# Kernel optimization log

Measured on AMD Instinct MI355X. Metric: run time of the kernel, lower is better.

The kernel has to match this reference:

```python
import jax, jax.numpy as jnp
import numpy as np

B, NUM_RX, NUM_CHIRPS, SAMPLES = 16, 4, 64, 256
D_BINS, R_BINS = 64, 256


def _conv3d(x, w, b, pad):
    y = jax.lax.conv_general_dilated(x, w, (1, 1, 1), pad,
                                     dimension_numbers=('NCDHW', 'OIDHW', 'NCDHW'))
    return y + b[None, :, None, None, None]


def _conv2d(x, w, b, pad):
    y = jax.lax.conv_general_dilated(x, w, (1, 1), pad,
                                     dimension_numbers=('NCHW', 'OIHW', 'NCHW'))
    return y + b[None, :, None, None]


def _bn2(x, s, t):
    return x * s[None, :, None, None] + t[None, :, None, None]


def _bn3(x, s, t):
    return x * s[None, :, None, None, None] + t[None, :, None, None, None]


def _upsample_bilinear_ac(x, oh, ow):
    # torch Upsample(mode='bilinear', align_corners=True)
    _, _, h, w = x.shape
    ph = jnp.linspace(0.0, h - 1.0, oh)
    pw = jnp.linspace(0.0, w - 1.0, ow)
    h0 = jnp.clip(jnp.floor(ph).astype(jnp.int32), 0, h - 1)
    h1 = jnp.clip(h0 + 1, 0, h - 1)
    fh = ph - h0
    w0 = jnp.clip(jnp.floor(pw).astype(jnp.int32), 0, w - 1)
    w1 = jnp.clip(w0 + 1, 0, w - 1)
    fw = pw - w0
    x = x[:, :, h0, :] * (1.0 - fh)[None, None, :, None] + x[:, :, h1, :] * fh[None, None, :, None]
    x = x[:, :, :, w0] * (1.0 - fw) + x[:, :, :, w1] * fw
    return x


def setup_inputs() -> dict:
    ks = iter(jax.random.split(jax.random.key(0), 80))

    def nrm(shape, s=0.05):
        return s * jax.random.normal(next(ks), shape, dtype=jnp.float32)

    inp = {'x': jax.random.normal(next(ks), (B, NUM_RX, NUM_CHIRPS, SAMPLES, 2), dtype=jnp.float32)}

    def conv(name, shape):
        inp[name + '_w'] = nrm(shape)
        inp[name + '_b'] = nrm((shape[0],))

    def bn(name, n):  # BatchNorm in inference form folded to scale/shift
        inp[name + '_s'] = 1.0 + nrm((n,), 0.1)
        inp[name + '_t'] = nrm((n,), 0.1)

    conv('tc1', (16, 2, 1, 1, 3)); bn('tc1', 16)
    conv('tc2', (32, 16, 1, 1, 3)); bn('tc2', 32)
    conv('rx', (32, 32, NUM_RX, 1, 1)); bn('rx', 32)
    conv('cc1', (64, 32 * NUM_CHIRPS, 3, 3)); bn('cc1', 64)
    conv('cc2', (64, 64, 3, 3)); bn('cc2', 64)
    conv('rd1', (128, 64, 3, 3)); bn('rd1', 128)
    conv('rd2', (128, 128, 3, 3)); bn('rd2', 128)
    conv('up1', (64, 128, 3, 3)); bn('up1', 64)
    conv('up2', (32, 64, 3, 3)); bn('up2', 32)
    conv('up3', (1, 32, 1, 1))
    inp['wr'] = jax.random.normal(next(ks), (SAMPLES, R_BINS, 2), dtype=jnp.float32)
    inp['wd'] = jax.random.normal(next(ks), (NUM_CHIRPS, D_BINS, 2), dtype=jnp.float32)
    return inp


def reference(x, tc1_w, tc1_b, tc1_s, tc1_t, tc2_w, tc2_b, tc2_s, tc2_t,
              rx_w, rx_b, rx_s, rx_t, cc1_w, cc1_b, cc1_s, cc1_t,
              cc2_w, cc2_b, cc2_s, cc2_t, rd1_w, rd1_b, rd1_s, rd1_t,
              rd2_w, rd2_b, rd2_s, rd2_t, up1_w, up1_b, up1_s, up1_t,
              up2_w, up2_b, up2_s, up2_t, up3_w, up3_b, wr, wd):
    r = jax.nn.relu
    p3 = [(0, 0), (0, 0), (1, 1)]
    p2 = [(1, 1), (1, 1)]
    h = jnp.transpose(x, (0, 4, 1, 2, 3))                      # [B,2,RX,C,S]
    h = r(_bn3(_conv3d(h, tc1_w, tc1_b, p3), tc1_s, tc1_t))
    h = r(_bn3(_conv3d(h, tc2_w, tc2_b, p3), tc2_s, tc2_t))
    h = r(_bn3(_conv3d(h, rx_w, rx_b, [(0, 0)] * 3), rx_s, rx_t))[:, :, 0]  # [B,32,C,S]
    h = h.reshape(h.shape[0], -1, SAMPLES)[:, :, None, :]      # [B,32*C,1,S]
    h = r(_bn2(_conv2d(h, cc1_w, cc1_b, p2), cc1_s, cc1_t))
    h = r(_bn2(_conv2d(h, cc2_w, cc2_b, p2), cc2_s, cc2_t))
    h = r(_bn2(_conv2d(h, rd1_w, rd1_b, p2), rd1_s, rd1_t))
    h = r(_bn2(_conv2d(h, rd2_w, rd2_b, p2), rd2_s, rd2_t))
    h = _upsample_bilinear_ac(h, D_BINS, R_BINS)               # [B,128,D,R]
    h = r(_bn2(_conv2d(h, up1_w, up1_b, p2), up1_s, up1_t))
    h = r(_bn2(_conv2d(h, up2_w, up2_b, p2), up2_s, up2_t))
    h = jax.nn.sigmoid(_conv2d(h, up3_w, up3_b, [(0, 0), (0, 0)]))  # [B,1,D,R]
    # learnable_fft (input is real: x_imag = 0), loops -> two batched matmuls
    xr = h[:, 0]                                               # [B,D,R]
    rr = jnp.einsum('bcs,sr->bcr', xr, wr[:, :, 0])            # range DFT, real
    ri = jnp.einsum('bcs,sr->bcr', xr, wr[:, :, 1])            # range DFT, imag
    rdr = jnp.einsum('bcr,cd->bdr', rr, wd[:, :, 0]) - jnp.einsum('bcr,cd->bdr', ri, wd[:, :, 1])
    rdi = jnp.einsum('bcr,cd->bdr', rr, wd[:, :, 1]) + jnp.einsum('bcr,cd->bdr', ri, wd[:, :, 0])
    mag = jnp.sqrt(rdr * rdr + rdi * rdi) / (NUM_CHIRPS * SAMPLES)
    out = jnp.clip(h + 0.1 * mag[:, None], 0.0, 1.0)
    return jnp.transpose(out, (0, 2, 3, 1))                    # [B,D,R,1]
```

## Files before the change

kernel.cpp:

```cpp
#include <hip/hip_runtime.h>
#include <math.h>

#define OFF_A      0u
#define OFF_P      8388608u
#define OFF_WCC1   10485760u
#define OFF_BCC1   11010048u
#define OFF_WCC2   11010112u
#define OFF_BCC2   11026496u
#define OFF_WRD1   11026560u
#define OFF_BRD1   11059328u
#define OFF_WRD2   11059456u
#define OFF_BRD2   11124992u
#define OFF_WUP1   11125120u
#define OFF_BUP1   11223424u
#define OFF_WUP2   11223488u
#define OFF_BUP2   11346368u
#define OFF_WRX    11346400u
#define OFF_R      0u
#define OFF_U1     524288u
#define OFF_H      1310720u

__device__ __forceinline__ void fma4(float4& a, const float4& x, float w) {
  a.x = fmaf(x.x, w, a.x); a.y = fmaf(x.y, w, a.y);
  a.z = fmaf(x.z, w, a.z); a.w = fmaf(x.w, w, a.w);
}

__global__ __launch_bounds__(256) void k_repack(
    const float* __restrict__ rx_w, const float* __restrict__ rx_s,
    const float* __restrict__ cc1_w, const float* __restrict__ cc1_b, const float* __restrict__ cc1_s, const float* __restrict__ cc1_t,
    const float* __restrict__ cc2_w, const float* __restrict__ cc2_b, const float* __restrict__ cc2_s, const float* __restrict__ cc2_t,
    const float* __restrict__ rd1_w, const float* __restrict__ rd1_b, const float* __restrict__ rd1_s, const float* __restrict__ rd1_t,
    const float* __restrict__ rd2_w, const float* __restrict__ rd2_b, const float* __restrict__ rd2_s, const float* __restrict__ rd2_t,
    const float* __restrict__ up1_w, const float* __restrict__ up1_b, const float* __restrict__ up1_s, const float* __restrict__ up1_t,
    const float* __restrict__ up2_w, const float* __restrict__ up2_b, const float* __restrict__ up2_s, const float* __restrict__ up2_t,
    float* __restrict__ ws)
{
  const int tid = blockIdx.x * blockDim.x + threadIdx.x;
  const int nth = gridDim.x * blockDim.x;

  for (int i = tid; i < 4096; i += nth) {
    int oc = i & 31, ic = (i >> 5) & 31, rxi = i >> 10;
    ws[OFF_WRX + i] = rx_w[(oc*32 + ic)*4 + rxi] * rx_s[oc];
  }

  for (int i = tid; i < 2048*64*4; i += nth) {
    int k = i & 3, oc = (i >> 2) & 63, c2 = i >> 8;
    ws[OFF_WCC1 + i] = (k < 3) ? cc1_w[((oc*2048 + c2)*3 + 1)*3 + k] * cc1_s[oc] : 0.f;
  }
  for (int i = tid; i < 64; i += nth) ws[OFF_BCC1 + i] = cc1_b[i]*cc1_s[i] + cc1_t[i];

  for (int i = tid; i < 64*64*4; i += nth) {
    int k = i & 3, oc = (i >> 2) & 63, ic = i >> 8;
    ws[OFF_WCC2 + i] = (k < 3) ? cc2_w[((oc*64 + ic)*3 + 1)*3 + k] * cc2_s[oc] : 0.f;
  }
  for (int i = tid; i < 64; i += nth) ws[OFF_BCC2 + i] = cc2_b[i]*cc2_s[i] + cc2_t[i];

  for (int i = tid; i < 64*128*4; i += nth) {
    int k = i & 3, oc = (i >> 2) & 127, ic = i >> 9;
    ws[OFF_WRD1 + i] = (k < 3) ? rd1_w[((oc*64 + ic)*3 + 1)*3 + k] * rd1_s[oc] : 0.f;
  }
  for (int i = tid; i < 128; i += nth) ws[OFF_BRD1 + i] = rd1_b[i]*rd1_s[i] + rd1_t[i];

  for (int i = tid; i < 128*128*4; i += nth) {
    int k = i & 3, oc = (i >> 2) & 127, ic = i >> 9;
    ws[OFF_WRD2 + i] = (k < 3) ? rd2_w[((oc*128 + ic)*3 + 1)*3 + k] * rd2_s[oc] : 0.f;
  }
  for (int i = tid; i < 128; i += nth) ws[OFF_BRD2 + i] = rd2_b[i]*rd2_s[i] + rd2_t[i];

  for (int i = tid; i < 3*128*64*4; i += nth) {
    int k = i & 3, oc = (i >> 2) & 63, ic = (i >> 8) & 127, v = i >> 15;
    float val = 0.f;
    if (k < 3) {
      const int m = (v == 0) ? 6 : (v == 1) ? 7 : 3;
      float a = 0.f;
      for (int kh = 0; kh < 3; ++kh)
        if ((m >> kh) & 1) a += up1_w[((oc*128 + ic)*3 + kh)*3 + k];
      val = a * up1_s[oc];
    }
    ws[OFF_WUP1 + i] = val;
  }
  for (int i = tid; i < 64; i += nth) ws[OFF_BUP1 + i] = up1_b[i]*up1_s[i] + up1_t[i];

  for (int i = tid; i < 5*3*64*32*4; i += nth) {
    int k = i & 3, oc = (i >> 2) & 31, ic = (i >> 7) & 63, t = i >> 13;
    int src = t % 3, v = t / 3;
    float val = 0.f;
    if (k < 3) {
      const int MASKS[15] = {2,4,0,  1,6,0,  0,7,0,  0,3,4,  0,1,2};
      const int m = MASKS[v*3 + src];
      float a = 0.f;
      for (int kh = 0; kh < 3; ++kh)
        if ((m >> kh) & 1) a += up2_w[((oc*64 + ic)*3 + kh)*3 + k];
      val = a * up2_s[oc];
    }
    ws[OFF_WUP2 + i] = val;
  }
  for (int i = tid; i < 32; i += nth) ws[OFF_BUP2 + i] = up2_b[i]*up2_s[i] + up2_t[i];
}

__global__ __launch_bounds__(256) void k_front(
    const float* __restrict__ x,
    const float* __restrict__ w1, const float* __restrict__ b1, const float* __restrict__ s1, const float* __restrict__ t1bn,
    const float* __restrict__ w2, const float* __restrict__ b2, const float* __restrict__ s2, const float* __restrict__ t2bn,
    const float* __restrict__ wrxF, const float* __restrict__ brx, const float* __restrict__ srx, const float* __restrict__ trx,
    float* __restrict__ A)
{
  __shared__ __align__(16) float t1s[16][256];
  __shared__ __align__(16) float t2s[16][256];
  __shared__ __align__(16) float w1f[16][6];
  __shared__ float b1f[16];
  __shared__ __align__(16) float w2t[16][3][32];
  __shared__ float b2f[32];
  __shared__ float brxf[32];

  const int tid = threadIdx.x;
  const int b = blockIdx.x >> 6, chirp = blockIdx.x & 63;

  if (tid < 96) (&w1f[0][0])[tid] = w1[tid] * s1[tid/6];
  if (tid < 16) b1f[tid] = b1[tid]*s1[tid] + t1bn[tid];
  for (int i = tid; i < 1536; i += 256) {
    int oc = i / 48, r = i - oc*48, ic = r / 3, k = r - ic*3;
    w2t[ic][k][oc] = w2[i] * s2[oc];
  }
  if (tid < 32) b2f[tid] = b2[tid]*s2[tid] + t2bn[tid];
  if (tid < 32) brxf[tid] = brx[tid]*srx[tid] + trx[tid];
  __syncthreads();

  const int s  = tid;
  const int sg = tid & 63;
  const int q  = tid >> 6;
  const int s0 = sg * 4;

  float4 acc[8];
  #pragma unroll
  for (int j = 0; j < 8; ++j) acc[j] = make_float4(0.f, 0.f, 0.f, 0.f);

  #pragma unroll 1
  for (int rxi = 0; rxi < 4; ++rxi) {
    {
      const float2* xb2 = (const float2*)(x + ((size_t)(((b*4 + rxi)*64 + chirp)*256) << 1));
      float2 xm = xb2[s];
      float2 xl = xb2[(s == 0) ? 0 : (s - 1)];
      float2 xr = xb2[(s == 255) ? 255 : (s + 1)];
      if (s == 0)   { xl.x = 0.f; xl.y = 0.f; }
      if (s == 255) { xr.x = 0.f; xr.y = 0.f; }
      #pragma unroll 4
      for (int o = 0; o < 16; ++o) {
        float v = b1f[o];
        v = fmaf(xl.x, w1f[o][0], v);
        v = fmaf(xm.x, w1f[o][1], v);
        v = fmaf(xr.x, w1f[o][2], v);
        v = fmaf(xl.y, w1f[o][3], v);
        v = fmaf(xm.y, w1f[o][4], v);
        v = fmaf(xr.y, w1f[o][5], v);
        t1s[o][s] = fmaxf(v, 0.f);
      }
    }
    __syncthreads();

    #pragma unroll 1
    for (int h = 0; h < 2; ++h) {
      {
        const int ocb = h*16 + q*4;
        float4 t2a[4];
        #pragma unroll
        for (int j = 0; j < 4; ++j) {
          float bv = b2f[ocb + j];
          t2a[j] = make_float4(bv, bv, bv, bv);
        }
        #pragma unroll 4
        for (int ic = 0; ic < 16; ++ic) {
          float4 tm = *(const float4*)&t1s[ic][s0];
          float tl = t1s[ic][(sg == 0) ? 0 : (s0 - 1)];
          float tr = t1s[ic][(sg == 63) ? 255 : (s0 + 4)];
          if (sg == 0)  tl = 0.f;
          if (sg == 63) tr = 0.f;
          float4 win0 = make_float4(tl, tm.x, tm.y, tm.z);
          float4 win2 = make_float4(tm.y, tm.z, tm.w, tr);
          float4 wA = *(const float4*)&w2t[ic][0][ocb];
          float4 wB = *(const float4*)&w2t[ic][1][ocb];
          float4 wC = *(const float4*)&w2t[ic][2][ocb];
          fma4(t2a[0], win0, wA.x); fma4(t2a[0], tm, wB.x); fma4(t2a[0], win2, wC.x);
          fma4(t2a[1], win0, wA.y); fma4(t2a[1], tm, wB.y); fma4(t2a[1], win2, wC.y);
          fma4(t2a[2], win0, wA.z); fma4(t2a[2], tm, wB.z); fma4(t2a[2], win2, wC.z);
          fma4(t2a[3], win0, wA.w); fma4(t2a[3], tm, wB.w); fma4(t2a[3], win2, wC.w);
        }
        #pragma unroll
        for (int j = 0; j < 4; ++j) {
          float4 r;
          r.x = fmaxf(t2a[j].x, 0.f); r.y = fmaxf(t2a[j].y, 0.f);
          r.z = fmaxf(t2a[j].z, 0.f); r.w = fmaxf(t2a[j].w, 0.f);
          *(float4*)&t2s[q*4 + j][s0] = r;
        }
      }
      __syncthreads();

      {
        const float* wbase = wrxF + ((rxi*32 + h*16)*32) + q*8;
        #pragma unroll 8
        for (int ic = 0; ic < 16; ++ic) {
          float4 tv = *(const float4*)&t2s[ic][s0];
          float4 wa = *(const float4*)(wbase + ic*32);
          float4 wb = *(const float4*)(wbase + ic*32 + 4);
          fma4(acc[0], tv, wa.x); fma4(acc[1], tv, wa.y);
          fma4(acc[2], tv, wa.z); fma4(acc[3], tv, wa.w);
          fma4(acc[4], tv, wb.x); fma4(acc[5], tv, wb.y);
          fma4(acc[6], tv, wb.z); fma4(acc[7], tv, wb.w);
        }
      }
      __syncthreads();
    }
  }

  #pragma unroll
  for (int j = 0; j < 8; ++j) {
    int oc = q*8 + j;
    float bb = brxf[oc];
    float4 r;
    r.x = fmaxf(acc[j].x + bb, 0.f); r.y = fmaxf(acc[j].y + bb, 0.f);
    r.z = fmaxf(acc[j].z + bb, 0.f); r.w = fmaxf(acc[j].w + bb, 0.f);
    *(float4*)&A[(size_t)((b*2048 + oc*64 + chirp)*256) + s0] = r;
  }
}

__global__ __launch_bounds__(256) void k_cc1(
    const float* __restrict__ A, const float* __restrict__ wp, float* __restrict__ P)
{
  __shared__ __align__(16) float As[256][36];
  const int tid = threadIdx.x;
  const int ks = blockIdx.x & 7;
  const int stile = (blockIdx.x >> 3) & 7;
  const int b = blockIdx.x >> 6;
  const int s0 = stile * 32;
  const int oc = tid & 63;
  const int sg = tid >> 6;
  const int cbase = ks * 256;
  const float4* w4 = (const float4*)wp;

  for (int i = tid; i < 256*36; i += 256) {
    int c = i / 36, si = i - c*36;
    int sA = s0 - 1 + si;
    float v = 0.f;
    if (si < 34 && sA >= 0 && sA < 256)
      v = A[(size_t)(b*2048 + cbase + c)*256 + sA];
    As[c][si] = v;
  }
  __syncthreads();

  const int sb = sg * 8;
  float4 acc0 = make_float4(0.f,0.f,0.f,0.f);
  float4 acc1 = make_float4(0.f,0.f,0.f,0.f);
  #pragma unroll 4
  for (int c = 0; c < 256; ++c) {
    float4 w = w4[(size_t)(cbase + c)*64 + oc];
    float4 a0 = *(const float4*)&As[c][sb];
    float4 a1 = *(const float4*)&As[c][sb + 4];
    float2 a2 = *(const float2*)&As[c][sb + 8];
    acc0.x = fmaf(a0.x,w.x, fmaf(a0.y,w.y, fmaf(a0.z,w.z, acc0.x)));
    acc0.y = fmaf(a0.y,w.x, fmaf(a0.z,w.y, fmaf(a0.w,w.z, acc0.y)));
    acc0.z = fmaf(a0.z,w.x, fmaf(a0.w,w.y, fmaf(a1.x,w.z, acc0.z)));
    acc0.w = fmaf(a0.w,w.x, fmaf(a1.x,w.y, fmaf(a1.y,w.z, acc0.w)));
    acc1.x = fmaf(a1.x,w.x, fmaf(a1.y,w.y, fmaf(a1.z,w.z, acc1.x)));
    acc1.y = fmaf(a1.y,w.x, fmaf(a1.z,w.y, fmaf(a1.w,w.z, acc1.y)));
    acc1.z = fmaf(a1.z,w.x, fmaf(a1.w,w.y, fmaf(a2.x,w.z, acc1.z)));
    acc1.w = fmaf(a1.w,w.x, fmaf(a2.x,w.y, fmaf(a2.y,w.z, acc1.w)));
  }
  float* Pk = P + ((size_t)(ks*16 + b)*256)*64;
  int s = s0 + sb;
  Pk[(size_t)(s+0)*64 + oc] = acc0.x;
  Pk[(size_t)(s+1)*64 + oc] = acc0.y;
  Pk[(size_t)(s+2)*64 + oc] = acc0.z;
  Pk[(size_t)(s+3)*64 + oc] = acc0.w;
  Pk[(size_t)(s+4)*64 + oc] = acc1.x;
  Pk[(size_t)(s+5)*64 + oc] = acc1.y;
  Pk[(size_t)(s+6)*64 + oc] = acc1.z;
  Pk[(size_t)(s+7)*64 + oc] = acc1.w;
}

__global__ __launch_bounds__(256) void k_mid(
    const float* __restrict__ P, const float* __restrict__ bcc1,
    const float* __restrict__ wcc2, const float* __restrict__ bcc2,
    const float* __restrict__ wrd1, const float* __restrict__ brd1,
    const float* __restrict__ wrd2, const float* __restrict__ brd2,
    float* __restrict__ R)
{
  __shared__ float c1s[14][64];
  __shared__ float c2s[14][64];
  __shared__ float r1s[10][128];
  const int tid = threadIdx.x;
  const int b = blockIdx.x >> 5;
  const int s0 = (blockIdx.x & 31) * 8;
  const float4* wc2 = (const float4*)wcc2;
  const float4* wr1 = (const float4*)wrd1;
  const float4* wr2 = (const float4*)wrd2;

  for (int i = tid; i < 14*64; i += 256) {
    int si = i >> 6, ic = i & 63;
    int sA = s0 - 3 + si;
    float v = 0.f;
    if (sA >= 0 && sA < 256) {
      float a = bcc1[ic];
      #pragma unroll
      for (int ksp = 0; ksp < 8; ++ksp)
        a += P[((size_t)(ksp*16 + b)*256 + sA)*64 + ic];
      v = fmaxf(a, 0.f);
    }
    c1s[si][ic] = v;
  }
  __syncthreads();

  {
    const int g = tid >> 6, oc = tid & 63;
    if (g < 3) {
      float4 acc;
      float bb = bcc2[oc];
      acc = make_float4(bb, bb, bb, bb);
      for (int ic = 0; ic < 64; ++ic) {
        float4 w = wc2[ic*64 + oc];
        float c0 = c1s[g*4+0][ic], c1 = c1s[g*4+1][ic], c2 = c1s[g*4+2][ic];
        float c3 = c1s[g*4+3][ic], c4 = c1s[g*4+4][ic], c5 = c1s[g*4+5][ic];
        acc.x = fmaf(c0,w.x, fmaf(c1,w.y, fmaf(c2,w.z, acc.x)));
        acc.y = fmaf(c1,w.x, fmaf(c2,w.y, fmaf(c3,w.z, acc.y)));
        acc.z = fmaf(c2,w.x, fmaf(c3,w.y, fmaf(c4,w.z, acc.z)));
        acc.w = fmaf(c3,w.x, fmaf(c4,w.y, fmaf(c5,w.z, acc.w)));
      }
      c2s[g*4+0][oc] = fmaxf(acc.x, 0.f);
      c2s[g*4+1][oc] = fmaxf(acc.y, 0.f);
      c2s[g*4+2][oc] = fmaxf(acc.z, 0.f);
      c2s[g*4+3][oc] = fmaxf(acc.w, 0.f);
    } else {
      int k = tid - 192;
      c2s[12][k] = 0.f;
      c2s[13][k] = 0.f;
    }
  }
  __syncthreads();

  for (int it = tid; it < 384; it += 256) {
    const int oc = it & 127, g = it >> 7;
    float4 acc;
    float bb = brd1[oc];
    acc = make_float4(bb, bb, bb, bb);
    for (int ic = 0; ic < 64; ++ic) {
      float4 w = wr1[ic*128 + oc];
      float c0 = c2s[g*4+0][ic], c1 = c2s[g*4+1][ic], c2 = c2s[g*4+2][ic];
      float c3 = c2s[g*4+3][ic], c4 = c2s[g*4+4][ic], c5 = c2s[g*4+5][ic];
      acc.x = fmaf(c0,w.x, fmaf(c1,w.y, fmaf(c2,w.z, acc.x)));
      acc.y = fmaf(c1,w.x, fmaf(c2,w.y, fmaf(c3,w.z, acc.y)));
      acc.z = fmaf(c2,w.x, fmaf(c3,w.y, fmaf(c4,w.z, acc.z)));
      acc.w = fmaf(c3,w.x, fmaf(c4,w.y, fmaf(c5,w.z, acc.w)));
    }
    r1s[g*4+0][oc] = fmaxf(acc.x, 0.f);
    r1s[g*4+1][oc] = fmaxf(acc.y, 0.f);
    if (g < 2) {
      r1s[g*4+2][oc] = fmaxf(acc.z, 0.f);
      r1s[g*4+3][oc] = fmaxf(acc.w, 0.f);
    }
  }
  __syncthreads();

  {
    const int g = tid >> 7, oc = tid & 127;
    float4 acc;
    float bb = brd2[oc];
    acc = make_float4(bb, bb, bb, bb);
    for (int ic = 0; ic < 128; ++ic) {
      float4 w = wr2[ic*128 + oc];
      float c0 = r1s[g*4+0][ic], c1 = r1s[g*4+1][ic], c2 = r1s[g*4+2][ic];
      float c3 = r1s[g*4+3][ic], c4 = r1s[g*4+4][ic], c5 = r1s[g*4+5][ic];
      acc.x = fmaf(c0,w.x, fmaf(c1,w.y, fmaf(c2,w.z, acc.x)));
      acc.y = fmaf(c1,w.x, fmaf(c2,w.y, fmaf(c3,w.z, acc.y)));
      acc.z = fmaf(c2,w.x, fmaf(c3,w.y, fmaf(c4,w.z, acc.z)));
      acc.w = fmaf(c3,w.x, fmaf(c4,w.y, fmaf(c5,w.z, acc.w)));
    }
    int s = s0 + g*4;
    R[((size_t)b*256 + s+0)*128 + oc] = fmaxf(acc.x, 0.f);
    R[((size_t)b*256 + s+1)*128 + oc] = fmaxf(acc.y, 0.f);
    R[((size_t)b*256 + s+2)*128 + oc] = fmaxf(acc.z, 0.f);
    R[((size_t)b*256 + s+3)*128 + oc] = fmaxf(acc.w, 0.f);
  }
}

__global__ __launch_bounds__(192) void k_up1(
    const float* __restrict__ R, const float* __restrict__ wup1, const float* __restrict__ bup1,
    float* __restrict__ U1)
{
  __shared__ float Rs[10][128];
  const int tid = threadIdx.x;
  const int b = blockIdx.x >> 5;
  const int s0 = (blockIdx.x & 31) * 8;
  for (int i = tid; i < 10*128; i += 192) {
    int si = i >> 7, ic = i & 127;
    int sA = s0 - 1 + si;
    Rs[si][ic] = (sA >= 0 && sA < 256) ? R[((size_t)b*256 + sA)*128 + ic] : 0.f;
  }
  __syncthreads();
  const int vi = tid >> 6, oc = tid & 63;
  const float4* w4 = (const float4*)wup1;
  float acc[8];
  float bb = bup1[oc];
  #pragma unroll
  for (int j = 0; j < 8; ++j) acc[j] = bb;
  for (int ic = 0; ic < 128; ++ic) {
    float4 w = w4[(vi*128 + ic)*64 + oc];
    float r0 = Rs[0][ic], r1 = Rs[1][ic], r2 = Rs[2][ic], r3 = Rs[3][ic], r4 = Rs[4][ic];
    float r5 = Rs[5][ic], r6 = Rs[6][ic], r7 = Rs[7][ic], r8 = Rs[8][ic], r9 = Rs[9][ic];
    acc[0] = fmaf(r0,w.x, fmaf(r1,w.y, fmaf(r2,w.z, acc[0])));
    acc[1] = fmaf(r1,w.x, fmaf(r2,w.y, fmaf(r3,w.z, acc[1])));
    acc[2] = fmaf(r2,w.x, fmaf(r3,w.y, fmaf(r4,w.z, acc[2])));
    acc[3] = fmaf(r3,w.x, fmaf(r4,w.y, fmaf(r5,w.z, acc[3])));
    acc[4] = fmaf(r4,w.x, fmaf(r5,w.y, fmaf(r6,w.z, acc[4])));
    acc[5] = fmaf(r5,w.x, fmaf(r6,w.y, fmaf(r7,w.z, acc[5])));
    acc[6] = fmaf(r6,w.x, fmaf(r7,w.y, fmaf(r8,w.z, acc[6])));
    acc[7] = fmaf(r7,w.x, fmaf(r8,w.y, fmaf(r9,w.z, acc[7])));
  }
  #pragma unroll
  for (int j = 0; j < 8; ++j)
    U1[((size_t)(b*3 + vi)*256 + s0 + j)*64 + oc] = fmaxf(acc[j], 0.f);
}

__global__ __launch_bounds__(192) void k_up2(
    const float* __restrict__ U1, const float* __restrict__ wup2, const float* __restrict__ bup2,
    const float* __restrict__ up3_w, const float* __restrict__ up3_b,
    float* __restrict__ H)
{
  __shared__ float u1s[3][10][64];
  __shared__ float u2s[5][32][9];
  const int tid = threadIdx.x;
  const int b = blockIdx.x >> 5;
  const int s0 = (blockIdx.x & 31) * 8;
  for (int i = tid; i < 3*10*64; i += 192) {
    int v = i / 640, r = i - v*640, si = r >> 6, ic = r & 63;
    int sA = s0 - 1 + si;
    u1s[v][si][ic] = (sA >= 0 && sA < 256) ? U1[((size_t)(b*3 + v)*256 + sA)*64 + ic] : 0.f;
  }
  __syncthreads();
  if (tid < 160) {
    const int v = tid >> 5, oc = tid & 31;
    const float4* w4 = (const float4*)wup2;
    float acc[8];
    float bb = bup2[oc];
    #pragma unroll
    for (int j = 0; j < 8; ++j) acc[j] = bb;
    for (int src = 0; src < 3; ++src)
      for (int ic = 0; ic < 64; ++ic) {
        float4 w = w4[((v*3 + src)*64 + ic)*32 + oc];
        float r0 = u1s[src][0][ic], r1 = u1s[src][1][ic], r2 = u1s[src][2][ic];
        float r3 = u1s[src][3][ic], r4 = u1s[src][4][ic], r5 = u1s[src][5][ic];
        float r6 = u1s[src][6][ic], r7 = u1s[src][7][ic], r8 = u1s[src][8][ic];
        float r9 = u1s[src][9][ic];
        acc[0] = fmaf(r0,w.x, fmaf(r1,w.y, fmaf(r2,w.z, acc[0])));
        acc[1] = fmaf(r1,w.x, fmaf(r2,w.y, fmaf(r3,w.z, acc[1])));
        acc[2] = fmaf(r2,w.x, fmaf(r3,w.y, fmaf(r4,w.z, acc[2])));
        acc[3] = fmaf(r3,w.x, fmaf(r4,w.y, fmaf(r5,w.z, acc[3])));
        acc[4] = fmaf(r4,w.x, fmaf(r5,w.y, fmaf(r6,w.z, acc[4])));
        acc[5] = fmaf(r5,w.x, fmaf(r6,w.y, fmaf(r7,w.z, acc[5])));
        acc[6] = fmaf(r6,w.x, fmaf(r7,w.y, fmaf(r8,w.z, acc[6])));
        acc[7] = fmaf(r7,w.x, fmaf(r8,w.y, fmaf(r9,w.z, acc[7])));
      }
    #pragma unroll
    for (int j = 0; j < 8; ++j) u2s[v][oc][j] = fmaxf(acc[j], 0.f);
  }
  __syncthreads();
  if (tid < 40) {
    int v = tid >> 3, j = tid & 7;
    float a = up3_b[0];
    for (int ic = 0; ic < 32; ++ic)
      a = fmaf(u2s[v][ic][j], up3_w[ic], a);
    H[(size_t)(b*5 + v)*256 + s0 + j] = 1.f / (1.f + expf(-a));
  }
}

__global__ __launch_bounds__(64) void k_spec(
    const float* __restrict__ H, const float* __restrict__ wr, const float* __restrict__ wd,
    float* __restrict__ out)
{
  __shared__ float hs[5][256];
  __shared__ float S0[64], S1[64];
  __shared__ float wds[4][64][2];
  const int tid = threadIdx.x;
  const int b = blockIdx.x >> 2;
  const int rt = blockIdx.x & 3;
  for (int i = tid; i < 1280; i += 64) hs[i >> 8][i & 255] = H[(size_t)b*1280 + i];
  {
    float a0 = 0.f, a1 = 0.f;
    for (int c = 2; c <= 61; ++c) {
      a0 += wd[(c*64 + tid)*2 + 0];
      a1 += wd[(c*64 + tid)*2 + 1];
    }
    S0[tid] = a0; S1[tid] = a1;
  }
  for (int i = tid; i < 512; i += 64) {
    int row = i >> 7, rem = i & 127, d = rem >> 1, comp = rem & 1;
    int c = (row < 2) ? row : (60 + row);
    wds[row][d][comp] = wd[(c*64 + d)*2 + comp];
  }
  __syncthreads();
  const int r = rt*64 + tid;
  float rr0=0,rr1=0,rr2=0,rr3=0,rr4=0, ri0=0,ri1=0,ri2=0,ri3=0,ri4=0;
  const float2* wr2p = (const float2*)wr;
  for (int s = 0; s < 256; ++s) {
    float2 w = wr2p[s*256 + r];
    float h0 = hs[0][s], h1 = hs[1][s], h2 = hs[2][s], h3 = hs[3][s], h4 = hs[4][s];
    rr0 = fmaf(h0, w.x, rr0); ri0 = fmaf(h0, w.y, ri0);
    rr1 = fmaf(h1, w.x, rr1); ri1 = fmaf(h1, w.y, ri1);
    rr2 = fmaf(h2, w.x, rr2); ri2 = fmaf(h2, w.y, ri2);
    rr3 = fmaf(h3, w.x, rr3); ri3 = fmaf(h3, w.y, ri3);
    rr4 = fmaf(h4, w.x, rr4); ri4 = fmaf(h4, w.y, ri4);
  }
  for (int d = 0; d < 64; ++d) {
    float w0r = wds[0][d][0], w0i = wds[0][d][1];
    float w1r = wds[1][d][0], w1i = wds[1][d][1];
    float w2r = wds[2][d][0], w2i = wds[2][d][1];
    float w3r = wds[3][d][0], w3i = wds[3][d][1];
    float s0v = S0[d], s1v = S1[d];
    float rdr = rr0*w0r + rr1*w1r + rr2*s0v + rr3*w2r + rr4*w3r
              - ri0*w0i - ri1*w1i - ri2*s1v - ri3*w2i - ri4*w3i;
    float rdi = rr0*w0i + rr1*w1i + rr2*s1v + rr3*w2i + rr4*w3i
              + ri0*w0r + ri1*w1r + ri2*s0v + ri3*w2r + ri4*w3r;
    float mag = sqrtf(rdr*rdr + rdi*rdi) * (1.0f / 16384.0f);
    int v = (d == 0) ? 0 : (d == 1) ? 1 : (d <= 61) ? 2 : ((d == 62) ? 3 : 4);
    float o = hs[v][r] + 0.1f * mag;
    out[(size_t)b*16384 + d*256 + r] = fminf(fmaxf(o, 0.f), 1.f);
  }
}

extern "C" void kernel_launch(void* const* d_in, const int* in_sizes, int n_in,
                              void* d_out, int out_size, void* d_ws, size_t ws_size,
                              hipStream_t stream)
{
  const float* x     = (const float*)d_in[0];
  const float* tc1_w = (const float*)d_in[1];  const float* tc1_b = (const float*)d_in[2];
  const float* tc1_s = (const float*)d_in[3];  const float* tc1_t = (const float*)d_in[4];
  const float* tc2_w = (const float*)d_in[5];  const float* tc2_b = (const float*)d_in[6];
  const float* tc2_s = (const float*)d_in[7];  const float* tc2_t = (const float*)d_in[8];
  const float* rx_w  = (const float*)d_in[9];  const float* rx_b  = (const float*)d_in[10];
  const float* rx_s  = (const float*)d_in[11]; const float* rx_t  = (const float*)d_in[12];
  const float* cc1_w = (const float*)d_in[13]; const float* cc1_b = (const float*)d_in[14];
  const float* cc1_s = (const float*)d_in[15]; const float* cc1_t = (const float*)d_in[16];
  const float* cc2_w = (const float*)d_in[17]; const float* cc2_b = (const float*)d_in[18];
  const float* cc2_s = (const float*)d_in[19]; const float* cc2_t = (const float*)d_in[20];
  const float* rd1_w = (const float*)d_in[21]; const float* rd1_b = (const float*)d_in[22];
  const float* rd1_s = (const float*)d_in[23]; const float* rd1_t = (const float*)d_in[24];
  const float* rd2_w = (const float*)d_in[25]; const float* rd2_b = (const float*)d_in[26];
  const float* rd2_s = (const float*)d_in[27]; const float* rd2_t = (const float*)d_in[28];
  const float* up1_w = (const float*)d_in[29]; const float* up1_b = (const float*)d_in[30];
  const float* up1_s = (const float*)d_in[31]; const float* up1_t = (const float*)d_in[32];
  const float* up2_w = (const float*)d_in[33]; const float* up2_b = (const float*)d_in[34];
  const float* up2_s = (const float*)d_in[35]; const float* up2_t = (const float*)d_in[36];
  const float* up3_w = (const float*)d_in[37]; const float* up3_b = (const float*)d_in[38];
  const float* wr    = (const float*)d_in[39];
  const float* wd    = (const float*)d_in[40];
  float* ws  = (float*)d_ws;
  float* out = (float*)d_out;

  k_repack<<<1024, 256, 0, stream>>>(rx_w, rx_s,
                                     cc1_w, cc1_b, cc1_s, cc1_t,
                                     cc2_w, cc2_b, cc2_s, cc2_t,
                                     rd1_w, rd1_b, rd1_s, rd1_t,
                                     rd2_w, rd2_b, rd2_s, rd2_t,
                                     up1_w, up1_b, up1_s, up1_t,
                                     up2_w, up2_b, up2_s, up2_t, ws);
  k_front<<<1024, 256, 0, stream>>>(x, tc1_w, tc1_b, tc1_s, tc1_t,
                                    tc2_w, tc2_b, tc2_s, tc2_t,
                                    ws + OFF_WRX, rx_b, rx_s, rx_t, ws + OFF_A);
  k_cc1<<<1024, 256, 0, stream>>>(ws + OFF_A, ws + OFF_WCC1, ws + OFF_P);
  k_mid<<<512, 256, 0, stream>>>(ws + OFF_P, ws + OFF_BCC1,
                                 ws + OFF_WCC2, ws + OFF_BCC2,
                                 ws + OFF_WRD1, ws + OFF_BRD1,
                                 ws + OFF_WRD2, ws + OFF_BRD2, ws + OFF_R);
  k_up1<<<512, 192, 0, stream>>>(ws + OFF_R, ws + OFF_WUP1, ws + OFF_BUP1, ws + OFF_U1);
  k_up2<<<512, 192, 0, stream>>>(ws + OFF_U1, ws + OFF_WUP2, ws + OFF_BUP2, up3_w, up3_b, ws + OFF_H);
  k_spec<<<64, 64, 0, stream>>>(ws + OFF_H, wr, wd, out);
}
```

Baseline: 420.4 us.

## Restructure k_front to per-thread register tiles with uniform weight loads

Moves the tc1/tc2/rx weight and bias folding into k_repack so k_front no longer prepares weights in shared memory per block. Each thread now owns one sample and keeps all 32 tc2 outputs and 32 rx accumulators in registers, reading weights from global memory with wave-uniform addresses (scalar loads) instead of staging t2 through shared memory. This removes the t2s shared buffer and several barriers per rxi iteration, at the cost of higher register pressure and scalar-load traffic. It also sets launch_bounds(256,4).

Measured after the change: 392.7 us. 1.07x faster.

```diff
diff --git a/kernel.cpp b/kernel.cpp
--- a/kernel.cpp
+++ b/kernel.cpp
@@ -16,6 +16,11 @@
 #define OFF_WUP2   11223488u
 #define OFF_BUP2   11346368u
 #define OFF_WRX    11346400u
+#define OFF_W1F    11350496u
+#define OFF_B1F    11350592u
+#define OFF_W2F    11350608u
+#define OFF_B2F    11352144u
+#define OFF_BRXF   11352176u
 #define OFF_R      0u
 #define OFF_U1     524288u
 #define OFF_H      1310720u
@@ -26,7 +31,9 @@
 }
 
 __global__ __launch_bounds__(256) void k_repack(
-    const float* __restrict__ rx_w, const float* __restrict__ rx_s,
+    const float* __restrict__ tc1_w, const float* __restrict__ tc1_b, const float* __restrict__ tc1_s, const float* __restrict__ tc1_t,
+    const float* __restrict__ tc2_w, const float* __restrict__ tc2_b, const float* __restrict__ tc2_s, const float* __restrict__ tc2_t,
+    const float* __restrict__ rx_w, const float* __restrict__ rx_b, const float* __restrict__ rx_s, const float* __restrict__ rx_t,
     const float* __restrict__ cc1_w, const float* __restrict__ cc1_b, const float* __restrict__ cc1_s, const float* __restrict__ cc1_t,
     const float* __restrict__ cc2_w, const float* __restrict__ cc2_b, const float* __restrict__ cc2_s, const float* __restrict__ cc2_t,
     const float* __restrict__ rd1_w, const float* __restrict__ rd1_b, const float* __restrict__ rd1_s, const float* __restrict__ rd1_t,
@@ -38,10 +45,18 @@
   const int tid = blockIdx.x * blockDim.x + threadIdx.x;
   const int nth = gridDim.x * blockDim.x;
 
+  for (int i = tid; i < 96; i += nth) ws[OFF_W1F + i] = tc1_w[i] * tc1_s[i/6];
+  for (int i = tid; i < 16; i += nth) ws[OFF_B1F + i] = tc1_b[i]*tc1_s[i] + tc1_t[i];
+  for (int i = tid; i < 1536; i += nth) {
+    int oc = i & 31, r = i >> 5, k = r % 3, ic = r / 3;
+    ws[OFF_W2F + i] = tc2_w[oc*48 + ic*3 + k] * tc2_s[oc];
+  }
+  for (int i = tid; i < 32; i += nth) ws[OFF_B2F + i] = tc2_b[i]*tc2_s[i] + tc2_t[i];
   for (int i = tid; i < 4096; i += nth) {
     int oc = i & 31, ic = (i >> 5) & 31, rxi = i >> 10;
     ws[OFF_WRX + i] = rx_w[(oc*32 + ic)*4 + rxi] * rx_s[oc];
   }
+  for (int i = tid; i < 32; i += nth) ws[OFF_BRXF + i] = rx_b[i]*rx_s[i] + rx_t[i];
 
   for (int i = tid; i < 2048*64*4; i += nth) {
     int k = i & 3, oc = (i >> 2) & 63, c2 = i >> 8;
@@ -98,42 +113,26 @@
   for (int i = tid; i < 32; i += nth) ws[OFF_BUP2 + i] = up2_b[i]*up2_s[i] + up2_t[i];
 }
 
-__global__ __launch_bounds__(256) void k_front(
-    const float* __restrict__ x,
-    const float* __restrict__ w1, const float* __restrict__ b1, const float* __restrict__ s1, const float* __restrict__ t1bn,
-    const float* __restrict__ w2, const float* __restrict__ b2, const float* __restrict__ s2, const float* __restrict__ t2bn,
-    const float* __restrict__ wrxF, const float* __restrict__ brx, const float* __restrict__ srx, const float* __restrict__ trx,
-    float* __restrict__ A)
-{
-  __shared__ __align__(16) float t1s[16][256];
-  __shared__ __align__(16) float t2s[16][256];
-  __shared__ __align__(16) float w1f[16][6];
-  __shared__ float b1f[16];
-  __shared__ __align__(16) float w2t[16][3][32];
-  __shared__ float b2f[32];
-  __shared__ float brxf[32];
-
+__global__ __launch_bounds__(256, 4) void k_front(
+    const float* __restrict__ x, const float* __restrict__ ws, float* __restrict__ A)
+{
+  __shared__ float t1s[16][258];
   const int tid = threadIdx.x;
   const int b = blockIdx.x >> 6, chirp = blockIdx.x & 63;
-
-  if (tid < 96) (&w1f[0][0])[tid] = w1[tid] * s1[tid/6];
-  if (tid < 16) b1f[tid] = b1[tid]*s1[tid] + t1bn[tid];
-  for (int i = tid; i < 1536; i += 256) {
-    int oc = i / 48, r = i - oc*48, ic = r / 3, k = r - ic*3;
-    w2t[ic][k][oc] = w2[i] * s2[oc];
-  }
-  if (tid < 32) b2f[tid] = b2[tid]*s2[tid] + t2bn[tid];
-  if (tid < 32) brxf[tid] = brx[tid]*srx[tid] + trx[tid];
-  __syncthreads();
-
-  const int s  = tid;
-  const int sg = tid & 63;
-  const int q  = tid >> 6;
-  const int s0 = sg * 4;
-
-  float4 acc[8];
+  const int s = tid;
+
+  if (tid < 32) { int o = tid & 15; int c = (tid >> 4) ? 257 : 0; t1s[o][c] = 0.f; }
+
+  const float* w1f  = ws + OFF_W1F;
+  const float* b1f  = ws + OFF_B1F;
+  const float* w2f  = ws + OFF_W2F;
+  const float* b2f  = ws + OFF_B2F;
+  const float* wrxf = ws + OFF_WRX;
+  const float* brxf = ws + OFF_BRXF;
+
+  float acc[32];
   #pragma unroll
-  for (int j = 0; j < 8; ++j) acc[j] = make_float4(0.f, 0.f, 0.f, 0.f);
+  for (int j = 0; j < 32; ++j) acc[j] = 0.f;
 
   #pragma unroll 1
   for (int rxi = 0; rxi < 4; ++rxi) {
@@ -146,80 +145,51 @@
       if (s == 255) { xr.x = 0.f; xr.y = 0.f; }
       #pragma unroll 4
       for (int o = 0; o < 16; ++o) {
+        const float* w = w1f + o*6;
         float v = b1f[o];
-        v = fmaf(xl.x, w1f[o][0], v);
-        v = fmaf(xm.x, w1f[o][1], v);
-        v = fmaf(xr.x, w1f[o][2], v);
-        v = fmaf(xl.y, w1f[o][3], v);
-        v = fmaf(xm.y, w1f[o][4], v);
-        v = fmaf(xr.y, w1f[o][5], v);
-        t1s[o][s] = fmaxf(v, 0.f);
+        v = fmaf(xl.x, w[0], v);
+        v = fmaf(xm.x, w[1], v);
+        v = fmaf(xr.x, w[2], v);
+        v = fmaf(xl.y, w[3], v);
+        v = fmaf(xm.y, w[4], v);
+        v = fmaf(xr.y, w[5], v);
+        t1s[o][s+1] = fmaxf(v, 0.f);
       }
     }
     __syncthreads();
 
-    #pragma unroll 1
-    for (int h = 0; h < 2; ++h) {
-      {
-        const int ocb = h*16 + q*4;
-        float4 t2a[4];
-        #pragma unroll
-        for (int j = 0; j < 4; ++j) {
-          float bv = b2f[ocb + j];
-          t2a[j] = make_float4(bv, bv, bv, bv);
-        }
-        #pragma unroll 4
-        for (int ic = 0; ic < 16; ++ic) {
-          float4 tm = *(const float4*)&t1s[ic][s0];
-          float tl = t1s[ic][(sg == 0) ? 0 : (s0 - 1)];
-          float tr = t1s[ic][(sg == 63) ? 255 : (s0 + 4)];
-          if (sg == 0)  tl = 0.f;
-          if (sg == 63) tr = 0.f;
-          float4 win0 = make_float4(tl, tm.x, tm.y, tm.z);
-          float4 win2 = make_float4(tm.y, tm.z, tm.w, tr);
-          float4 wA = *(const float4*)&w2t[ic][0][ocb];
-          float4 wB = *(const float4*)&w2t[ic][1][ocb];
-          float4 wC = *(const float4*)&w2t[ic][2][ocb];
-          fma4(t2a[0], win0, wA.x); fma4(t2a[0], tm, wB.x); fma4(t2a[0], win2, wC.x);
-          fma4(t2a[1], win0, wA.y); fma4(t2a[1], tm, wB.y); fma4(t2a[1], win2, wC.y);
-          fma4(t2a[2], win0, wA.z); fma4(t2a[2], tm, wB.z); fma4(t2a[2], win2, wC.z);
-          fma4(t2a[3], win0, wA.w); fma4(t2a[3], tm, wB.w); fma4(t2a[3], win2, wC.w);
-        }
-        #pragma unroll
-        for (int j = 0; j < 4; ++j) {
-          float4 r;
-          r.x = fmaxf(t2a[j].x, 0.f); r.y = fmaxf(t2a[j].y, 0.f);
-          r.z = fmaxf(t2a[j].z, 0.f); r.w = fmaxf(t2a[j].w, 0.f);
-          *(float4*)&t2s[q*4 + j][s0] = r;
-        }
-      }
-      __syncthreads();
-
-      {
-        const float* wbase = wrxF + ((rxi*32 + h*16)*32) + q*8;
-        #pragma unroll 8
-        for (int ic = 0; ic < 16; ++ic) {
-          float4 tv = *(const float4*)&t2s[ic][s0];
-          float4 wa = *(const float4*)(wbase + ic*32);
-          float4 wb = *(const float4*)(wbase + ic*32 + 4);
-          fma4(acc[0], tv, wa.x); fma4(acc[1], tv, wa.y);
-          fma4(acc[2], tv, wa.z); fma4(acc[3], tv, wa.w);
-          fma4(acc[4], tv, wb.x); fma4(acc[5], tv, wb.y);
-          fma4(acc[6], tv, wb.z); fma4(acc[7], tv, wb.w);
-        }
-      }
-      __syncthreads();
-    }
-  }
-
-  #pragma unroll
-  for (int j = 0; j < 8; ++j) {
-    int oc = q*8 + j;
-    float bb = brxf[oc];
-    float4 r;
-    r.x = fmaxf(acc[j].x + bb, 0.f); r.y = fmaxf(acc[j].y + bb, 0.f);
-    r.z = fmaxf(acc[j].z + bb, 0.f); r.w = fmaxf(acc[j].w + bb, 0.f);
-    *(float4*)&A[(size_t)((b*2048 + oc*64 + chirp)*256) + s0] = r;
+    float t2[32];
+    #pragma unroll
+    for (int j = 0; j < 32; ++j) t2[j] = b2f[j];
+    #pragma unroll 2
+    for (int ic = 0; ic < 16; ++ic) {
+      float tl = t1s[ic][s];
+      float tm = t1s[ic][s+1];
+      float tr = t1s[ic][s+2];
+      const float* w = w2f + ic*96;
+      #pragma unroll
+      for (int oc = 0; oc < 32; ++oc)
+        t2[oc] = fmaf(tl, w[oc], fmaf(tm, w[32+oc], fmaf(tr, w[64+oc], t2[oc])));
+    }
+    #pragma unroll
+    for (int j = 0; j < 32; ++j) t2[j] = fmaxf(t2[j], 0.f);
+
+    const float* wr0 = wrxf + rxi*1024;
+    #pragma unroll 4
+    for (int ic = 0; ic < 32; ++ic) {
+      float tv = t2[ic];
+      const float* w = wr0 + ic*32;
+      #pragma unroll
+      for (int oc = 0; oc < 32; ++oc)
+        acc[oc] = fmaf(tv, w[oc], acc[oc]);
+    }
+    __syncthreads();
+  }
+
+  #pragma unroll 4
+  for (int oc = 0; oc < 32; ++oc) {
+    float v = fmaxf(acc[oc] + brxf[oc], 0.f);
+    A[(size_t)((b*2048 + oc*64 + chirp)*256) + s] = v;
   }
 }
 
@@ -554,16 +524,16 @@
   float* ws  = (float*)d_ws;
   float* out = (float*)d_out;
 
-  k_repack<<<1024, 256, 0, stream>>>(rx_w, rx_s,
+  k_repack<<<1024, 256, 0, stream>>>(tc1_w, tc1_b, tc1_s, tc1_t,
+                                     tc2_w, tc2_b, tc2_s, tc2_t,
+                                     rx_w, rx_b, rx_s, rx_t,
                                      cc1_w, cc1_b, cc1_s, cc1_t,
                                      cc2_w, cc2_b, cc2_s, cc2_t,
                                      rd1_w, rd1_b, rd1_s, rd1_t,
                                      rd2_w, rd2_b, rd2_s, rd2_t,
                                      up1_w, up1_b, up1_s, up1_t,
                                      up2_w, up2_b, up2_s, up2_t, ws);
-  k_front<<<1024, 256, 0, stream>>>(x, tc1_w, tc1_b, tc1_s, tc1_t,
-                                    tc2_w, tc2_b, tc2_s, tc2_t,
-                                    ws + OFF_WRX, rx_b, rx_s, rx_t, ws + OFF_A);
+  k_front<<<1024, 256, 0, stream>>>(x, ws, ws + OFF_A);
   k_cc1<<<1024, 256, 0, stream>>>(ws + OFF_A, ws + OFF_WCC1, ws + OFF_P);
   k_mid<<<512, 256, 0, stream>>>(ws + OFF_P, ws + OFF_BCC1,
                                  ws + OFF_WCC2, ws + OFF_BCC2,
```
